# Optimization experiments

Hardware: AMD Instinct MI355X
Metric: run time of the kernel (lower is better)

Reference implementation:

```python
import jax, jax.numpy as jnp
import numpy as np

B = 4_194_304

def setup_inputs() -> dict:
    key = jax.random.key(0)
    k1, k2, k3, k4, k5 = jax.random.split(key, 5)
    return {
        "pred": jax.random.normal(k1, (B, 2), dtype=jnp.float32),
        "target": jax.random.normal(k2, (B, 1), dtype=jnp.float32),
        "prev_pci": jax.random.normal(k3, (B, 1), dtype=jnp.float32),
        "delta_time": jax.random.randint(k4, (B,), 0, 10, dtype=jnp.int32),
        "pv_values": jax.random.randint(k5, (B,), 0, 2, dtype=jnp.int32),
    }

def reference(pred, target, prev_pci, delta_time, pv_values):
    # pred: [B,2] -> lower/upper interval bounds, kept as [B,1] columns
    lower = pred[:, 0:1]
    upper = pred[:, 1:2]
    center = (lower + upper) * 0.5                    # [B,1]

    center_loss = jnp.mean((target - center) ** 2)
    width_loss = jnp.mean(upper - lower)
    valid_penalty = jnp.mean(jnp.maximum(lower - upper, 0.0))

    # Vectorized form of the per-sample conditional penalty:
    #   pv==0 & dt!=0 -> relu(center - prev)
    #   pv!=0 & dt!=0 -> relu(prev - center)
    #   dt==0         -> 0
    dt_nz = (delta_time != 0)[:, None]                # [B,1]
    pv_zero = (pv_values == 0)[:, None]               # [B,1]
    pen_up = jax.nn.relu(center - prev_pci)
    pen_dn = jax.nn.relu(prev_pci - center)
    per_sample = jnp.where(dt_nz & pv_zero, pen_up,
                  jnp.where(dt_nz & ~pv_zero, pen_dn, 0.0))
    direction_penalty = jnp.sum(per_sample)

    n = pv_values.shape[0]
    total = (center_loss * 1.5 + 0.1 * width_loss
             + 10.0 * valid_penalty + 0.5 * direction_penalty / n)
    return total
```

## Files before the change

### kernel.cpp

```cpp
#include <hip/hip_runtime.h>

#define THREADS 256
#define WAVE 64

__global__ __launch_bounds__(THREADS) void loss_reduce(
    const float4* __restrict__ pred4,
    const float4* __restrict__ tgt4,
    const float4* __restrict__ prev4,
    const int4*   __restrict__ dt4,
    const int4*   __restrict__ pv4,
    float4* __restrict__ partials,
    int n4)
{
    int i = blockIdx.x * THREADS + threadIdx.x;
    float s0 = 0.f, s1 = 0.f, s2 = 0.f, s3 = 0.f;
    if (i < n4) {
        float4 p0 = pred4[2 * i];
        float4 p1 = pred4[2 * i + 1];
        float4 tg = tgt4[i];
        float4 pp = prev4[i];
        int4   dt = dt4[i];
        int4   pv = pv4[i];

        float lo[4] = {p0.x, p0.z, p1.x, p1.z};
        float up[4] = {p0.y, p0.w, p1.y, p1.w};
        float tga[4] = {tg.x, tg.y, tg.z, tg.w};
        float ppa[4] = {pp.x, pp.y, pp.z, pp.w};
        int dta[4] = {dt.x, dt.y, dt.z, dt.w};
        int pva[4] = {pv.x, pv.y, pv.z, pv.w};

#pragma unroll
        for (int j = 0; j < 4; ++j) {
            float c = 0.5f * (lo[j] + up[j]);
            float d = tga[j] - c;
            s0 += d * d;
            s1 += up[j] - lo[j];
            s2 += fmaxf(lo[j] - up[j], 0.0f);
            float diff = c - ppa[j];
            float pen = (pva[j] == 0) ? fmaxf(diff, 0.0f) : fmaxf(-diff, 0.0f);
            s3 += (dta[j] != 0) ? pen : 0.0f;
        }
    }

#pragma unroll
    for (int off = 32; off > 0; off >>= 1) {
        s0 += __shfl_down(s0, off, WAVE);
        s1 += __shfl_down(s1, off, WAVE);
        s2 += __shfl_down(s2, off, WAVE);
        s3 += __shfl_down(s3, off, WAVE);
    }

    __shared__ float4 smem[THREADS / WAVE];
    int wave = threadIdx.x >> 6;
    if ((threadIdx.x & 63) == 0) smem[wave] = make_float4(s0, s1, s2, s3);
    __syncthreads();
    if (threadIdx.x == 0) {
        float4 acc = smem[0];
#pragma unroll
        for (int w = 1; w < THREADS / WAVE; ++w) {
            acc.x += smem[w].x; acc.y += smem[w].y;
            acc.z += smem[w].z; acc.w += smem[w].w;
        }
        partials[blockIdx.x] = acc;
    }
}

__global__ __launch_bounds__(THREADS) void loss_final(
    const float4* __restrict__ partials, int nblocks,
    const float* __restrict__ pred, const float* __restrict__ tgt,
    const float* __restrict__ prev, const int* __restrict__ dt,
    const int* __restrict__ pvv,
    int tail_start, int n,
    float* __restrict__ out)
{
    float s0 = 0.f, s1 = 0.f, s2 = 0.f, s3 = 0.f;
    for (int t = threadIdx.x; t < nblocks; t += THREADS) {
        float4 p = partials[t];
        s0 += p.x; s1 += p.y; s2 += p.z; s3 += p.w;
    }
    if (threadIdx.x == 0) {
        for (int i = tail_start; i < n; ++i) {
            float lo = pred[2 * i], up = pred[2 * i + 1];
            float c = 0.5f * (lo + up);
            float d = tgt[i] - c;
            s0 += d * d; s1 += up - lo; s2 += fmaxf(lo - up, 0.f);
            float diff = c - prev[i];
            float pen = (pvv[i] == 0) ? fmaxf(diff, 0.f) : fmaxf(-diff, 0.f);
            s3 += (dt[i] != 0) ? pen : 0.f;
        }
    }

#pragma unroll
    for (int off = 32; off > 0; off >>= 1) {
        s0 += __shfl_down(s0, off, WAVE);
        s1 += __shfl_down(s1, off, WAVE);
        s2 += __shfl_down(s2, off, WAVE);
        s3 += __shfl_down(s3, off, WAVE);
    }

    __shared__ float4 smem[THREADS / WAVE];
    int wave = threadIdx.x >> 6;
    if ((threadIdx.x & 63) == 0) smem[wave] = make_float4(s0, s1, s2, s3);
    __syncthreads();
    if (threadIdx.x == 0) {
        float4 acc = smem[0];
#pragma unroll
        for (int w = 1; w < THREADS / WAVE; ++w) {
            acc.x += smem[w].x; acc.y += smem[w].y;
            acc.z += smem[w].z; acc.w += smem[w].w;
        }
        float inv_n = 1.0f / (float)n;
        out[0] = (1.5f * acc.x + 0.1f * acc.y + 10.0f * acc.z + 0.5f * acc.w) * inv_n;
    }
}

extern "C" void kernel_launch(void* const* d_in, const int* in_sizes, int n_in,
                              void* d_out, int out_size, void* d_ws, size_t ws_size,
                              hipStream_t stream) {
    const float* pred   = (const float*)d_in[0];
    const float* target = (const float*)d_in[1];
    const float* prev   = (const float*)d_in[2];
    const int*   dt     = (const int*)d_in[3];
    const int*   pv     = (const int*)d_in[4];
    float* out = (float*)d_out;

    int n  = in_sizes[3];
    int n4 = n >> 2;
    int nblocks = (n4 + THREADS - 1) / THREADS;

    float4* partials = (float4*)d_ws;

    loss_reduce<<<nblocks, THREADS, 0, stream>>>(
        (const float4*)pred, (const float4*)target, (const float4*)prev,
        (const int4*)dt, (const int4*)pv, partials, n4);

    loss_final<<<1, THREADS, 0, stream>>>(
        partials, nblocks, pred, target, prev, dt, pv, n4 * 4, n, out);
}
```

Before: 124.9 us.

## Process two vector groups per thread and reduce a single weighted scalar

Each thread now loads two float4 groups up front before computing, which doubles the loads in flight per thread and halves the block count. The four separate accumulators are folded into one weighted scalar per thread before the wave and block reductions, so partials are one float per block instead of a float4. This cuts shuffle and shared-memory work and reduces the partial traffic and final-kernel reads. The trade-off is higher register use and a change in floating-point summation order.

New measurement: 121.4 us. -2.8%, faster.

```diff
diff --git a/kernel.cpp b/kernel.cpp
--- a/kernel.cpp
+++ b/kernel.cpp
@@ -2,6 +2,7 @@
 
 #define THREADS 256
 #define WAVE 64
+#define GROUPS_PER_BLOCK (THREADS * 2)
 
 __global__ __launch_bounds__(THREADS) void loss_reduce(
     const float4* __restrict__ pred4,
@@ -9,26 +10,62 @@
     const float4* __restrict__ prev4,
     const int4*   __restrict__ dt4,
     const int4*   __restrict__ pv4,
-    float4* __restrict__ partials,
+    float* __restrict__ partials,
     int n4)
 {
-    int i = blockIdx.x * THREADS + threadIdx.x;
+    int i0 = blockIdx.x * GROUPS_PER_BLOCK + threadIdx.x;
+    int i1 = i0 + THREADS;
+    bool v0 = (i0 < n4);
+    bool v1 = (i1 < n4);
+
+    float4 a0, a1, t0, q0;  int4 d0, e0;
+    float4 b0, b1, t1, q1;  int4 d1, e1;
+
+    if (v0) {
+        a0 = pred4[2 * i0];
+        a1 = pred4[2 * i0 + 1];
+        t0 = tgt4[i0];
+        q0 = prev4[i0];
+        d0 = dt4[i0];
+        e0 = pv4[i0];
+    }
+    if (v1) {
+        b0 = pred4[2 * i1];
+        b1 = pred4[2 * i1 + 1];
+        t1 = tgt4[i1];
+        q1 = prev4[i1];
+        d1 = dt4[i1];
+        e1 = pv4[i1];
+    }
+
     float s0 = 0.f, s1 = 0.f, s2 = 0.f, s3 = 0.f;
-    if (i < n4) {
-        float4 p0 = pred4[2 * i];
-        float4 p1 = pred4[2 * i + 1];
-        float4 tg = tgt4[i];
-        float4 pp = prev4[i];
-        int4   dt = dt4[i];
-        int4   pv = pv4[i];
 
-        float lo[4] = {p0.x, p0.z, p1.x, p1.z};
-        float up[4] = {p0.y, p0.w, p1.y, p1.w};
-        float tga[4] = {tg.x, tg.y, tg.z, tg.w};
-        float ppa[4] = {pp.x, pp.y, pp.z, pp.w};
-        int dta[4] = {dt.x, dt.y, dt.z, dt.w};
-        int pva[4] = {pv.x, pv.y, pv.z, pv.w};
-
+    if (v0) {
+        float lo[4]  = {a0.x, a0.z, a1.x, a1.z};
+        float up[4]  = {a0.y, a0.w, a1.y, a1.w};
+        float tga[4] = {t0.x, t0.y, t0.z, t0.w};
+        float ppa[4] = {q0.x, q0.y, q0.z, q0.w};
+        int   dta[4] = {d0.x, d0.y, d0.z, d0.w};
+        int   pva[4] = {e0.x, e0.y, e0.z, e0.w};
+#pragma unroll
+        for (int j = 0; j < 4; ++j) {
+            float c = 0.5f * (lo[j] + up[j]);
+            float d = tga[j] - c;
+            s0 += d * d;
+            s1 += up[j] - lo[j];
+            s2 += fmaxf(lo[j] - up[j], 0.0f);
+            float diff = c - ppa[j];
+            float pen = (pva[j] == 0) ? fmaxf(diff, 0.0f) : fmaxf(-diff, 0.0f);
+            s3 += (dta[j] != 0) ? pen : 0.0f;
+        }
+    }
+    if (v1) {
+        float lo[4]  = {b0.x, b0.z, b1.x, b1.z};
+        float up[4]  = {b0.y, b0.w, b1.y, b1.w};
+        float tga[4] = {t1.x, t1.y, t1.z, t1.w};
+        float ppa[4] = {q1.x, q1.y, q1.z, q1.w};
+        int   dta[4] = {d1.x, d1.y, d1.z, d1.w};
+        int   pva[4] = {e1.x, e1.y, e1.z, e1.w};
 #pragma unroll
         for (int j = 0; j < 4; ++j) {
             float c = 0.5f * (lo[j] + up[j]);
@@ -42,75 +79,59 @@
         }
     }
 
+    float w = 1.5f * s0 + 0.1f * s1 + 10.0f * s2 + 0.5f * s3;
+
 #pragma unroll
-    for (int off = 32; off > 0; off >>= 1) {
-        s0 += __shfl_down(s0, off, WAVE);
-        s1 += __shfl_down(s1, off, WAVE);
-        s2 += __shfl_down(s2, off, WAVE);
-        s3 += __shfl_down(s3, off, WAVE);
-    }
+    for (int off = 32; off > 0; off >>= 1)
+        w += __shfl_down(w, off, WAVE);
 
-    __shared__ float4 smem[THREADS / WAVE];
-    int wave = threadIdx.x >> 6;
-    if ((threadIdx.x & 63) == 0) smem[wave] = make_float4(s0, s1, s2, s3);
+    __shared__ float smem[THREADS / WAVE];
+    if ((threadIdx.x & 63) == 0) smem[threadIdx.x >> 6] = w;
     __syncthreads();
     if (threadIdx.x == 0) {
-        float4 acc = smem[0];
+        float acc = smem[0];
 #pragma unroll
-        for (int w = 1; w < THREADS / WAVE; ++w) {
-            acc.x += smem[w].x; acc.y += smem[w].y;
-            acc.z += smem[w].z; acc.w += smem[w].w;
-        }
+        for (int wv = 1; wv < THREADS / WAVE; ++wv) acc += smem[wv];
         partials[blockIdx.x] = acc;
     }
 }
 
 __global__ __launch_bounds__(THREADS) void loss_final(
-    const float4* __restrict__ partials, int nblocks,
+    const float* __restrict__ partials, int nblocks,
     const float* __restrict__ pred, const float* __restrict__ tgt,
     const float* __restrict__ prev, const int* __restrict__ dt,
     const int* __restrict__ pvv,
     int tail_start, int n,
     float* __restrict__ out)
 {
-    float s0 = 0.f, s1 = 0.f, s2 = 0.f, s3 = 0.f;
-    for (int t = threadIdx.x; t < nblocks; t += THREADS) {
-        float4 p = partials[t];
-        s0 += p.x; s1 += p.y; s2 += p.z; s3 += p.w;
-    }
+    float s = 0.f;
+    for (int t = threadIdx.x; t < nblocks; t += THREADS)
+        s += partials[t];
+
     if (threadIdx.x == 0) {
         for (int i = tail_start; i < n; ++i) {
             float lo = pred[2 * i], up = pred[2 * i + 1];
             float c = 0.5f * (lo + up);
             float d = tgt[i] - c;
-            s0 += d * d; s1 += up - lo; s2 += fmaxf(lo - up, 0.f);
-            float diff = c - prev[i];
-            float pen = (pvv[i] == 0) ? fmaxf(diff, 0.f) : fmaxf(-diff, 0.f);
-            s3 += (dt[i] != 0) ? pen : 0.f;
+            float pen = (pvv[i] == 0) ? fmaxf(c - prev[i], 0.f)
+                                      : fmaxf(prev[i] - c, 0.f);
+            s += 1.5f * d * d + 0.1f * (up - lo) + 10.0f * fmaxf(lo - up, 0.f)
+               + 0.5f * ((dt[i] != 0) ? pen : 0.f);
         }
     }
 
 #pragma unroll
-    for (int off = 32; off > 0; off >>= 1) {
-        s0 += __shfl_down(s0, off, WAVE);
-        s1 += __shfl_down(s1, off, WAVE);
-        s2 += __shfl_down(s2, off, WAVE);
-        s3 += __shfl_down(s3, off, WAVE);
-    }
+    for (int off = 32; off > 0; off >>= 1)
+        s += __shfl_down(s, off, WAVE);
 
-    __shared__ float4 smem[THREADS / WAVE];
-    int wave = threadIdx.x >> 6;
-    if ((threadIdx.x & 63) == 0) smem[wave] = make_float4(s0, s1, s2, s3);
+    __shared__ float smem[THREADS / WAVE];
+    if ((threadIdx.x & 63) == 0) smem[threadIdx.x >> 6] = s;
     __syncthreads();
     if (threadIdx.x == 0) {
-        float4 acc = smem[0];
+        float acc = smem[0];
 #pragma unroll
-        for (int w = 1; w < THREADS / WAVE; ++w) {
-            acc.x += smem[w].x; acc.y += smem[w].y;
-            acc.z += smem[w].z; acc.w += smem[w].w;
-        }
-        float inv_n = 1.0f / (float)n;
-        out[0] = (1.5f * acc.x + 0.1f * acc.y + 10.0f * acc.z + 0.5f * acc.w) * inv_n;
+        for (int wv = 1; wv < THREADS / WAVE; ++wv) acc += smem[wv];
+        out[0] = acc / (float)n;
     }
 }
 
@@ -126,9 +147,9 @@
 
     int n  = in_sizes[3];
     int n4 = n >> 2;
-    int nblocks = (n4 + THREADS - 1) / THREADS;
+    int nblocks = (n4 + GROUPS_PER_BLOCK - 1) / GROUPS_PER_BLOCK;
 
-    float4* partials = (float4*)d_ws;
+    float* partials = (float*)d_ws;
 
     loss_reduce<<<nblocks, THREADS, 0, stream>>>(
         (const float4*)pred, (const float4*)target, (const float4*)prev,
```
